# Kernel optimization log

Measured on AMD Instinct MI355X. Metric: run time of the kernel, lower is better.

Reference implementation:

```python
import jax, jax.numpy as jnp
import numpy as np

VERTS = [5023, 1256, 314, 79, 20]
SPIRAL_LEN = 9
T_FRAMES = 32
LATENT = 64


def _spiral_conv(x, idx, W, b):
    # x: [B, N, C]; idx: [N, L]; gather spiral neighborhoods then linear
    B = x.shape[0]
    g = x[:, idx.reshape(-1), :].reshape(B, idx.shape[0], -1)  # [B, N, L*C]
    return g @ W.T + b


def _pool(x, rows, cols, vals, n_out):
    # sparse matmul: out[b, rows] += x[b, cols] * vals  (index_select + scatter_add)
    gathered = x[:, cols, :] * vals[None, :, None]
    return jnp.zeros((x.shape[0], n_out, x.shape[2]), x.dtype).at[:, rows, :].add(gathered)


def _lstm_dir(x, Wih, Whh, bih, bhh, reverse):
    # x: [T, B, D]; PyTorch gate order i, f, g, o
    Bz, H = x.shape[1], Whh.shape[1]
    bias = bih + bhh
    def step(carry, xt):
        h, c = carry
        g = xt @ Wih.T + h @ Whh.T + bias
        i, f, gg, o = jnp.split(g, 4, axis=-1)
        c = jax.nn.sigmoid(f) * c + jax.nn.sigmoid(i) * jnp.tanh(gg)
        h = jax.nn.sigmoid(o) * jnp.tanh(c)
        return (h, c), h
    init = (jnp.zeros((Bz, H), x.dtype), jnp.zeros((Bz, H), x.dtype))
    _, hs = jax.lax.scan(step, init, x, reverse=reverse)
    return hs


def _forward(audio_hidden, vertices, actor,
             sp_idx0, sp_idx1, sp_idx2, sp_idx3,
             d0_rows, d0_cols, d0_vals, d1_rows, d1_cols, d1_vals,
             d2_rows, d2_cols, d2_vals, d3_rows, d3_cols, d3_vals,
             u0_rows, u0_cols, u0_vals, u1_rows, u1_cols, u1_vals,
             u2_rows, u2_cols, u2_vals, u3_rows, u3_cols, u3_vals,
             enc_W0, enc_b0, enc_W1, enc_b1, enc_W2, enc_b2, enc_W3, enc_b3,
             enc_lin_W, enc_lin_b, dec_lin_W, dec_lin_b,
             dec_W0, dec_b0, dec_W1, dec_b1, dec_W2, dec_b2, dec_W3, dec_b3,
             dec_W4, dec_b4, aud_W, aud_b,
             l0_Wih, l0_Whh, l0_bih, l0_bhh, l12_Wih, l12_Whh, l12_bih, l12_bhh):
    ah = audio_hidden
    if ah.shape[1] % 2 != 0:
        ah = ah[:, :ah.shape[1] - 1]
    tv = vertices.shape[1]
    if ah.shape[1] > 2 * tv:
        ah = ah[:, :2 * tv]
    elif ah.shape[1] < 2 * tv:
        tv = ah.shape[1] // 2
    hs = ah.reshape(1, ah.shape[1] // 2, ah.shape[2] * 2)[:, :tv]  # [1, T, 1536]
    audio_emb = hs @ aud_W.T + aud_b                                # [1, T, LATENT]
    # --- mesh encoder on actor template: (spiral conv -> ELU -> down pool) x4 -> Linear ---
    sp = (sp_idx0, sp_idx1, sp_idx2, sp_idx3)
    down = ((d0_rows, d0_cols, d0_vals), (d1_rows, d1_cols, d1_vals),
            (d2_rows, d2_cols, d2_vals), (d3_rows, d3_cols, d3_vals))
    encp = ((enc_W0, enc_b0), (enc_W1, enc_b1), (enc_W2, enc_b2), (enc_W3, enc_b3))
    x = actor
    for i in range(4):
        x = jax.nn.elu(_spiral_conv(x, sp[i], *encp[i]))
        x = _pool(x, *down[i], VERTS[i + 1])
    z = x.reshape(x.shape[0], -1) @ enc_lin_W.T + enc_lin_b        # [1, LATENT]
    actor_emb = jnp.broadcast_to(z[:, None, :], audio_emb.shape)
    # --- 3-layer bidirectional LSTM ---
    h = jnp.concatenate([audio_emb, actor_emb], axis=-1).transpose(1, 0, 2)  # [T, 1, 2*LATENT]
    for layer in range(3):
        if layer == 0:
            Wih, Whh, bih, bhh = l0_Wih, l0_Whh, l0_bih, l0_bhh
        else:
            Wih, Whh, bih, bhh = l12_Wih[layer - 1], l12_Whh[layer - 1], l12_bih[layer - 1], l12_bhh[layer - 1]
        f = _lstm_dir(h, Wih[0], Whh[0], bih[0], bhh[0], False)
        r = _lstm_dir(h, Wih[1], Whh[1], bih[1], bhh[1], True)
        h = jnp.concatenate([f, r], axis=-1)
    latent = h.transpose(1, 0, 2)[0]                               # [T, LATENT]
    # --- mesh decoder, batched over all frames (replaces the python per-frame loop) ---
    up = ((u0_rows, u0_cols, u0_vals), (u1_rows, u1_cols, u1_vals),
          (u2_rows, u2_cols, u2_vals), (u3_rows, u3_cols, u3_vals))
    decp = ((dec_W0, dec_b0), (dec_W1, dec_b1), (dec_W2, dec_b2), (dec_W3, dec_b3))
    y = latent @ dec_lin_W.T + dec_lin_b                           # [T, 20*256]
    y = y.reshape(y.shape[0], VERTS[4], -1)                        # [T, 20, 256]
    for i in range(4):
        j = 3 - i
        y = _pool(y, *up[j], VERTS[j])
        y = jax.nn.elu(_spiral_conv(y, sp[j], *decp[i]))
    y = _spiral_conv(y, sp[0], dec_W4, dec_b4)                     # [T, 5023, 3]
    return y + actor                                               # broadcast residual, == vstacked preds


def setup_inputs() -> dict:
    key = jax.random.key(0)
    ks = iter(jax.random.split(key, 96))
    def nrm(shape, s=0.05):
        return jax.random.normal(next(ks), shape, jnp.float32) * s
    def rint(shape, hi):
        return jax.random.randint(next(ks), shape, 0, hi)
    inp = {}
    inp['audio_hidden'] = nrm((1, 2 * T_FRAMES, 768), 1.0)
    inp['vertices'] = nrm((1, T_FRAMES, VERTS[0], 3), 1.0)
    inp['actor'] = nrm((1, VERTS[0], 3), 1.0)
    for i in range(4):
        inp['sp_idx%d' % i] = rint((VERTS[i], SPIRAL_LEN), VERTS[i])
    for i in range(4):
        nnz = 3 * VERTS[i + 1]
        inp['d%d_rows' % i] = rint((nnz,), VERTS[i + 1])
        inp['d%d_cols' % i] = rint((nnz,), VERTS[i])
        inp['d%d_vals' % i] = jax.random.uniform(next(ks), (nnz,), jnp.float32)
    for i in range(4):
        nnz = 3 * VERTS[i]
        inp['u%d_rows' % i] = rint((nnz,), VERTS[i])
        inp['u%d_cols' % i] = rint((nnz,), VERTS[i + 1])
        inp['u%d_vals' % i] = jax.random.uniform(next(ks), (nnz,), jnp.float32)
    OC = [32, 64, 128, 256]
    ic = 3
    for i in range(4):
        inp['enc_W%d' % i] = nrm((OC[i], ic * SPIRAL_LEN))
        inp['enc_b%d' % i] = nrm((OC[i],))
        ic = OC[i]
    inp['enc_lin_W'] = nrm((LATENT, VERTS[4] * OC[3]))
    inp['enc_lin_b'] = nrm((LATENT,))
    inp['dec_lin_W'] = nrm((VERTS[4] * OC[3], LATENT))
    inp['dec_lin_b'] = nrm((VERTS[4] * OC[3],))
    dic = [256, 256, 128, 64]
    doc = [256, 128, 64, 32]
    for i in range(4):
        inp['dec_W%d' % i] = nrm((doc[i], dic[i] * SPIRAL_LEN))
        inp['dec_b%d' % i] = nrm((doc[i],))
    inp['dec_W4'] = nrm((3, OC[0] * SPIRAL_LEN))
    inp['dec_b4'] = nrm((3,))
    inp['aud_W'] = nrm((LATENT, 1536))
    inp['aud_b'] = nrm((LATENT,))
    H = LATENT // 2
    inp['l0_Wih'] = nrm((2, 4 * H, 2 * LATENT))
    inp['l0_Whh'] = nrm((2, 4 * H, H))
    inp['l0_bih'] = nrm((2, 4 * H))
    inp['l0_bhh'] = nrm((2, 4 * H))
    inp['l12_Wih'] = nrm((2, 2, 4 * H, 2 * H))
    inp['l12_Whh'] = nrm((2, 2, 4 * H, H))
    inp['l12_bih'] = nrm((2, 2, 4 * H))
    inp['l12_bhh'] = nrm((2, 2, 4 * H))
    return inp


def reference(audio_hidden, vertices, actor,
              sp_idx0, sp_idx1, sp_idx2, sp_idx3,
              d0_rows, d0_cols, d0_vals, d1_rows, d1_cols, d1_vals,
              d2_rows, d2_cols, d2_vals, d3_rows, d3_cols, d3_vals,
              u0_rows, u0_cols, u0_vals, u1_rows, u1_cols, u1_vals,
              u2_rows, u2_cols, u2_vals, u3_rows, u3_cols, u3_vals,
              enc_W0, enc_b0, enc_W1, enc_b1, enc_W2, enc_b2, enc_W3, enc_b3,
              enc_lin_W, enc_lin_b, dec_lin_W, dec_lin_b,
              dec_W0, dec_b0, dec_W1, dec_b1, dec_W2, dec_b2, dec_W3, dec_b3,
              dec_W4, dec_b4, aud_W, aud_b,
              l0_Wih, l0_Whh, l0_bih, l0_bhh, l12_Wih, l12_Whh, l12_bih, l12_bhh):
    return _forward(audio_hidden, vertices, actor,
                    sp_idx0, sp_idx1, sp_idx2, sp_idx3,
                    d0_rows, d0_cols, d0_vals, d1_rows, d1_cols, d1_vals,
                    d2_rows, d2_cols, d2_vals, d3_rows, d3_cols, d3_vals,
                    u0_rows, u0_cols, u0_vals, u1_rows, u1_cols, u1_vals,
                    u2_rows, u2_cols, u2_vals, u3_rows, u3_cols, u3_vals,
                    enc_W0, enc_b0, enc_W1, enc_b1, enc_W2, enc_b2, enc_W3, enc_b3,
                    enc_lin_W, enc_lin_b, dec_lin_W, dec_lin_b,
                    dec_W0, dec_b0, dec_W1, dec_b1, dec_W2, dec_b2, dec_W3, dec_b3,
                    dec_W4, dec_b4, aud_W, aud_b,
                    l0_Wih, l0_Whh, l0_bih, l0_bhh, l12_Wih, l12_Whh, l12_bih, l12_bhh)
```

## Files before the change

kernel.cpp:

```cpp
#include <hip/hip_runtime.h>
#include <cstdint>
#include <cstddef>


typedef unsigned short u16;
typedef __attribute__((ext_vector_type(8))) short short8;
typedef __attribute__((ext_vector_type(4))) float float4v;
#define CDIV(a,b) (((a)+(b)-1)/(b))
#define POOL_CAP 64

__device__ __forceinline__ float bf(u16 u){ return __uint_as_float(((unsigned)u)<<16); }
__device__ __forceinline__ u16 fb(float x){
  unsigned u = __float_as_uint(x);
  unsigned r = u + 0x7fffu + ((u>>16)&1u);
  return (u16)(r>>16);
}
__device__ __forceinline__ float lo16(unsigned u){ return __uint_as_float(u<<16); }
__device__ __forceinline__ float hi16(unsigned u){ return __uint_as_float(u & 0xffff0000u); }

struct WCast { const float* src[7]; int cum[8]; };
struct Lists {
  const int* rows[8];
  int nnz[8];
  int curoff[8];
  int lstoff[8];
};

__global__ void __launch_bounds__(256) setup_k(
    Lists L, int totN, int NF, int* __restrict__ curBase, int* __restrict__ lstBase,
    WCast C, int totW, int NC, u16* __restrict__ Wbf,
    const float* __restrict__ audio, const float* __restrict__ audW,
    const float* __restrict__ audB, float* __restrict__ h0,
    const int* __restrict__ u3rows, const int* __restrict__ u3cols,
    const float* __restrict__ u3vals,
    const float* __restrict__ dlW, const float* __restrict__ dlb,
    float* __restrict__ M, float* __restrict__ bp, int NM){
  int blk = blockIdx.x;
  int tid = threadIdx.x;
  if (blk < NF){
    int i = blk*256 + tid;
    if (i < totN){
      int off = i, k = 0;
      while (off >= L.nnz[k]){ off -= L.nnz[k]; k++; }
      int r = L.rows[k][off];
      int p = atomicAdd(curBase + L.curoff[k] + r, 1);
      if (p < POOL_CAP) lstBase[L.lstoff[k] + r*POOL_CAP + p] = off;
    }
    return;
  }
  blk -= NF;
  if (blk < NC){
    int i = blk*256 + tid;
    if (i < totW){
      int k = 0;
      while (i >= C.cum[k+1]) k++;
      Wbf[i] = fb(C.src[k][i - C.cum[k]]);
    }
    return;
  }
  blk -= NC;
  if (blk < 32){
    int t = blk;
    int f = tid >> 2, sl = tid & 3;
    const float4* x4 = (const float4*)(audio + t*1536);
    const float4* w4 = (const float4*)(audW + f*1536);
    float acc = 0.f;
    for (int k=sl; k<384; k+=4){
      float4 xv = x4[k], wv = w4[k];
      acc += xv.x*wv.x + xv.y*wv.y + xv.z*wv.z + xv.w*wv.w;
    }
    acc += __shfl_down(acc, 2, 64);
    acc += __shfl_down(acc, 1, 64);
    if (sl == 0) h0[t*128 + f] = acc + audB[f];
    return;
  }
  blk -= 32;
  if (blk < NM){
    int i = blk*256 + tid;
    if (i >= 79*256*16) return;
    int k4 = i & 15; int rc = i >> 4;
    int c = rc & 255; int r = rc >> 8;
    float4 acc = {0.f,0.f,0.f,0.f};
    for (int e=0; e<237; ++e){
      if (u3rows[e] == r){
        float v = u3vals[e];
        float4 w = *(const float4*)(dlW + ((size_t)(u3cols[e]*256 + c))*64 + k4*4);
        acc.x += v*w.x; acc.y += v*w.y; acc.z += v*w.z; acc.w += v*w.w;
      }
    }
    *(float4*)(M + (size_t)rc*64 + k4*4) = acc;
    return;
  }
  blk -= NM;
  int i = blk*256 + tid;
  if (i >= 79*256) return;
  int c = i & 255; int r = i >> 8;
  float acc = 0.f;
  for (int e=0; e<237; ++e)
    if (u3rows[e] == r) acc += u3vals[e]*dlb[u3cols[e]*256 + c];
  bp[i] = acc;
}

__global__ void __launch_bounds__(256) fs1_k(
    const float* __restrict__ x, const int* __restrict__ sp,
    const int* __restrict__ cols, const float* __restrict__ vals,
    const int* __restrict__ cur, const int* __restrict__ lst,
    const float* __restrict__ W, const float* __restrict__ bias,
    u16* __restrict__ out){
  int i = blockIdx.x*256 + threadIdx.x;
  if (i >= 1256*32) return;
  int c = i & 31, r = i >> 5;
  int deg = cur[r]; if (deg > POOL_CAP) deg = POOL_CAP;
  const int* le = lst + r*POOL_CAP;
  float bc = bias[c];
  const float* wc = W + (size_t)c*27;
  float acc = 0.f;
  for (int k=0;k<deg;k++){
    int e = le[k];
    float v = vals[e];
    const int* vix = sp + cols[e]*9;
    float s = bc;
    #pragma unroll
    for (int j=0;j<9;j++){
      const float* xr = x + (size_t)vix[j]*3;
      s += xr[0]*wc[j*3] + xr[1]*wc[j*3+1] + xr[2]*wc[j*3+2];
    }
    if (s < 0.f) s = expm1f(s);
    acc += v*s;
  }
  out[i] = fb(acc);
}

template<int IC, int BN, int BM>
__global__ void __launch_bounds__(256) conv_mfma(
    const u16* __restrict__ x, const int* __restrict__ idx,
    const u16* __restrict__ Wb, const float* __restrict__ bias,
    u16* __restrict__ out, int V, int OC, int M){
  constexpr int K = 9*IC;
  constexpr int KC = K/32;
  constexpr int NT = BN/16;
  constexpr int MT = BM/64;
  constexpr int LOG2 = (IC==32?5: IC==64?6: IC==128?7:8);
  constexpr int AST = 40;
  __shared__ u16 Asm[2][BM*AST];
  __shared__ u16 Bsm[2][BN*AST];
  __shared__ int rowB[BM], rowV[BM];
  __shared__ int sidx[BM*9];
  int t = threadIdx.x;
  int m0 = blockIdx.x*BM;
  int o0 = blockIdx.y*BN;
  if (t < BM){
    int mg = m0 + t;
    if (mg < M){ int b = mg / V; rowB[t] = b; rowV[t] = mg - b*V; }
    else rowB[t] = -1;
  }
  __syncthreads();
  for (int i=t; i<BM*9; i+=256){
    int r = i/9, s = i - r*9;
    sidx[i] = (rowB[r] >= 0) ? idx[rowV[r]*9 + s] : 0;
  }
  int lane = t & 63, wave = t >> 6;
  int quad = lane >> 4, col = lane & 15;
  float4v acc[MT][NT];
  #pragma unroll
  for (int mi=0;mi<MT;mi++)
    #pragma unroll
    for (int nt=0;nt<NT;nt++) acc[mi][nt] = (float4v)0.f;

  uint4 aval[MT]; uint4 bval;
  auto fetch = [&](int kc){
    int s  = (kc*32) >> LOG2;
    int c0 = (kc*32) & (IC-1);
    #pragma unroll
    for (int rpt=0; rpt<MT; ++rpt){
      int seg = t + 256*rpt;
      int arow = seg >> 2, aq = seg & 3;
      int b = rowB[arow];
      uint4 v = {0u,0u,0u,0u};
      if (b >= 0){
        int ix = sidx[arow*9 + s];
        v = *(const uint4*)(x + ((size_t)b*V + ix)*IC + c0 + aq*8);
      }
      aval[rpt] = v;
    }
    if (t < BN*4){
      int br = t >> 2, bq = t & 3;
      bval = *(const uint4*)(Wb + (size_t)(o0+br)*K + kc*32 + bq*8);
    }
  };

  __syncthreads();
  fetch(0);

  for (int kc = 0; kc < KC; ++kc){
    int buf = kc & 1;
    #pragma unroll
    for (int rpt=0; rpt<MT; ++rpt){
      int seg = t + 256*rpt;
      int arow = seg >> 2, aq = seg & 3;
      *(uint4*)&Asm[buf][arow*AST + aq*8] = aval[rpt];
    }
    if (t < BN*4){
      int br = t >> 2, bq = t & 3;
      *(uint4*)&Bsm[buf][br*AST + bq*8] = bval;
    }
    __syncthreads();
    if (kc+1 < KC) fetch(kc+1);
    short8 a[MT];
    #pragma unroll
    for (int mi=0;mi<MT;mi++)
      a[mi] = *(const short8*)&Asm[buf][(wave*MT*16 + mi*16 + col)*AST + quad*8];
    #pragma unroll
    for (int nt=0; nt<NT; ++nt){
      short8 bfr = *(const short8*)&Bsm[buf][(nt*16 + col)*AST + quad*8];
      #pragma unroll
      for (int mi=0;mi<MT;mi++)
        acc[mi][nt] = __builtin_amdgcn_mfma_f32_16x16x32_bf16(a[mi], bfr, acc[mi][nt], 0, 0, 0);
    }
  }
  #pragma unroll
  for (int mi=0;mi<MT;mi++){
    #pragma unroll
    for (int nt=0; nt<NT; ++nt){
      int o = o0 + nt*16 + col;
      float bv = bias[o];
      #pragma unroll
      for (int r=0;r<4;r++){
        int mg = m0 + wave*MT*16 + mi*16 + quad*4 + r;
        if (mg < M){
          float val = acc[mi][nt][r] + bv;
          if (val < 0.f) val = expm1f(val);
          out[(size_t)mg*OC + o] = fb(val);
        }
      }
    }
  }
}

__global__ void pool_g8_k(const u16* __restrict__ x, const int* __restrict__ cols,
                          const float* __restrict__ vals, const int* __restrict__ cur,
                          const int* __restrict__ lst, u16* __restrict__ out,
                          int B, int Vin, int Vout, int C){
  int C8 = C >> 3;
  int total = B*Vout*C8;
  int i = blockIdx.x*blockDim.x + threadIdx.x;
  if (i >= total) return;
  int c8 = i % C8; int tt = i / C8; int r = tt % Vout; int b = tt / Vout;
  int deg = cur[r]; if (deg > POOL_CAP) deg = POOL_CAP;
  const int* le = lst + r*POOL_CAP;
  float a0=0.f,a1=0.f,a2=0.f,a3=0.f,a4=0.f,a5=0.f,a6=0.f,a7=0.f;
  for (int k=0;k<deg;k++){
    int e = le[k];
    float v = vals[e];
    uint4 xv = *(const uint4*)(x + ((size_t)b*Vin + (size_t)cols[e])*C + c8*8);
    a0 += v*lo16(xv.x); a1 += v*hi16(xv.x);
    a2 += v*lo16(xv.y); a3 += v*hi16(xv.y);
    a4 += v*lo16(xv.z); a5 += v*hi16(xv.z);
    a6 += v*lo16(xv.w); a7 += v*hi16(xv.w);
  }
  uint4 o;
  o.x = ((unsigned)fb(a0)) | (((unsigned)fb(a1))<<16);
  o.y = ((unsigned)fb(a2)) | (((unsigned)fb(a3))<<16);
  o.z = ((unsigned)fb(a4)) | (((unsigned)fb(a5))<<16);
  o.w = ((unsigned)fb(a6)) | (((unsigned)fb(a7))<<16);
  *(uint4*)(out + ((size_t)b*Vout + (size_t)r)*C + c8*8) = o;
}

__global__ void __launch_bounds__(256) enc_lin_k(
    const u16* __restrict__ x, const float* __restrict__ W,
    const float* __restrict__ b, float* __restrict__ h0){
  int f = blockIdx.x;
  int t = threadIdx.x;
  const ushort4* x4 = (const ushort4*)x;
  const float4* w4 = (const float4*)(W + (size_t)f*5120);
  float acc = 0.f;
  for (int k=t; k<1280; k+=256){
    ushort4 xv = x4[k]; float4 wv = w4[k];
    acc += bf(xv.x)*wv.x + bf(xv.y)*wv.y + bf(xv.z)*wv.z + bf(xv.w)*wv.w;
  }
  #pragma unroll
  for (int off=32; off; off>>=1) acc += __shfl_down(acc, off, 64);
  __shared__ float red[4];
  if ((t & 63) == 0) red[t>>6] = acc;
  __syncthreads();
  if (t < 32){
    float zf = b[f] + red[0] + red[1] + red[2] + red[3];
    h0[t*128 + 64 + f] = zf;
  }
}

__device__ __forceinline__ float sigm(float x){ return 1.f/(1.f+__expf(-x)); }
__device__ __forceinline__ float tanhfast(float x){ return 1.f - 2.f/(__expf(2.f*x)+1.f); }

__global__ void __launch_bounds__(256) lstm3_k(
    const float* __restrict__ h0,
    const float* __restrict__ l0_Wih, const float* __restrict__ l0_Whh,
    const float* __restrict__ l0_bih, const float* __restrict__ l0_bhh,
    const float* __restrict__ l12_Wih, const float* __restrict__ l12_Whh,
    const float* __restrict__ l12_bih, const float* __restrict__ l12_bhh,
    float* __restrict__ latent){
  __shared__ __align__(16) u16 xb[32*136];
  __shared__ __align__(16) float xp[2*32*128];
  __shared__ __align__(16) u16 obuf[32*64];
  __shared__ __align__(16) float hsh32[2][32];
  __shared__ float bias_l[256];
  int t = threadIdx.x;
  int lane = t & 63, wave = t >> 6;
  int quad = lane >> 4, col = lane & 15;

  for (int i=t;i<32*128;i+=256){ int tt=i>>7, k=i&127; xb[tt*136+k]=fb(h0[i]); }

  for (int layer=0; layer<3; layer++){
    int IN = (layer==0)?128:64;
    const float *Wih,*Whh,*bih,*bhh;
    if (layer==0){ Wih=l0_Wih; Whh=l0_Whh; bih=l0_bih; bhh=l0_bhh; }
    else {
      int mb=(layer-1)*2;
      Wih=l12_Wih + (size_t)mb*128*64; Whh=l12_Whh + (size_t)mb*128*32;
      bih=l12_bih + mb*128; bhh=l12_bhh + mb*128;
    }
    bias_l[t] = bih[(t>>7)*128 + (t&127)] + bhh[(t>>7)*128 + (t&127)];
    __syncthreads();

    {
      int dirA = wave >> 1, o0 = (wave & 1)*64;
      const float* WA = Wih + (size_t)dirA*128*IN;
      float4v acc[2][4];
      #pragma unroll
      for (int mi=0;mi<2;mi++)
        #pragma unroll
        for (int nt=0;nt<4;nt++) acc[mi][nt] = (float4v)0.f;
      for (int kc=0; kc<IN/32; ++kc){
        short8 bfrag[4];
        #pragma unroll
        for (int nt=0;nt<4;nt++){
          const float* src = WA + (size_t)(o0+nt*16+col)*IN + kc*32 + quad*8;
          float4 w0 = *(const float4*)src;
          float4 w1 = *(const float4*)(src+4);
          alignas(16) u16 tmp[8] = {fb(w0.x),fb(w0.y),fb(w0.z),fb(w0.w),
                                    fb(w1.x),fb(w1.y),fb(w1.z),fb(w1.w)};
          bfrag[nt] = *(const short8*)tmp;
        }
        short8 afrag[2];
        #pragma unroll
        for (int mi=0;mi<2;mi++)
          afrag[mi] = *(const short8*)&xb[(mi*16+col)*136 + kc*32 + quad*8];
        #pragma unroll
        for (int nt=0;nt<4;nt++)
          #pragma unroll
          for (int mi=0;mi<2;mi++)
            acc[mi][nt] = __builtin_amdgcn_mfma_f32_16x16x32_bf16(afrag[mi], bfrag[nt], acc[mi][nt], 0, 0, 0);
      }
      #pragma unroll
      for (int mi=0;mi<2;mi++)
        #pragma unroll
        for (int nt=0;nt<4;nt++){
          int j = o0 + nt*16 + col;
          float bv = bias_l[dirA*128 + j];
          #pragma unroll
          for (int r=0;r<4;r++){
            int tt = mi*16 + quad*4 + r;
            xp[dirA*4096 + tt*128 + j] = acc[mi][nt][r] + bv;
          }
        }
    }
    __syncthreads();

    if (wave < 2){
      int dir = wave; bool rev = (dir == 1);
      int unit = lane & 31, gh = lane >> 5;
      int jA = gh*32 + unit;
      int jB = (gh+2)*32 + unit;
      const float* WD = Whh + (size_t)dir*128*32;
      float wA[32], wB[32];
      #pragma unroll
      for (int k=0;k<32;k++){ wA[k]=WD[(size_t)jA*32+k]; wB[k]=WD[(size_t)jB*32+k]; }
      float* hsd = &hsh32[dir][0];
      if (gh==0) hsd[unit] = 0.f;
      float creg = 0.f;
      const float* xpd = xp + dir*4096;
      float gAc = xpd[(rev?31:0)*128 + jA];
      float gBc = xpd[(rev?31:0)*128 + jB];
      #pragma unroll 1
      for (int s=0;s<32;s++){
        int tx = rev ? (31-s) : s;
        int sn = (s+1 < 32) ? s+1 : 31;
        int txn = rev ? (31-sn) : sn;
        float gA2 = xpd[txn*128 + jA];
        float gB2 = xpd[txn*128 + jB];
        const float4* h4 = (const float4*)hsd;
        float a0=0.f,a1=0.f,a2=0.f,a3=0.f,b0=0.f,b1=0.f,b2=0.f,b3=0.f;
        #pragma unroll
        for (int k=0;k<8;k++){
          float4 hv = h4[k];
          a0=fmaf(hv.x,wA[4*k+0],a0); b0=fmaf(hv.x,wB[4*k+0],b0);
          a1=fmaf(hv.y,wA[4*k+1],a1); b1=fmaf(hv.y,wB[4*k+1],b1);
          a2=fmaf(hv.z,wA[4*k+2],a2); b2=fmaf(hv.z,wB[4*k+2],b2);
          a3=fmaf(hv.w,wA[4*k+3],a3); b3=fmaf(hv.w,wB[4*k+3],b3);
        }
        float gA = gAc + ((a0+a1)+(a2+a3));
        float gB = gBc + ((b0+b1)+(b2+b3));
        float actA = sigm(gA);
        float tB = sigm(gh ? gB : 2.f*gB);
        float actB = gh ? tB : (2.f*tB - 1.f);
        float pA = __shfl_xor(actA, 32, 64);
        float pB = __shfl_xor(actB, 32, 64);
        float gi = gh ? pA : actA;
        float gf = gh ? actA : pA;
        float gg = gh ? pB : actB;
        float go = gh ? actB : pB;
        float cn = fmaf(gf, creg, gi*gg);
        float hn = go * tanhfast(cn);
        creg = cn;
        if (gh==0){
          hsd[unit] = hn;
          obuf[tx*64 + dir*32 + unit] = fb(hn);
        }
        gAc = gA2; gBc = gB2;
      }
    }
    __syncthreads();
    if (layer < 2){
      for (int i=t;i<32*64;i+=256){ int tt=i>>6, k=i&63; xb[tt*136+k]=obuf[i]; }
      __syncthreads();
    }
  }
  for (int i=t;i<32*64;i+=256) latent[i] = bf(obuf[i]);
}

__global__ void __launch_bounds__(256) dlp_k(
    const float* __restrict__ latent, const float* __restrict__ M,
    const float* __restrict__ bp, u16* __restrict__ y){
  __shared__ float mt[64][65];
  __shared__ float lt[32][64];
  int tid = threadIdx.x;
  int r = blockIdx.x % 79;
  int c0 = (blockIdx.x / 79) * 64;
  for (int i=tid; i<2048; i+=256) lt[i>>6][i&63] = latent[i];
  const float* Msrc = M + ((size_t)r*256 + c0)*64;
  for (int i=tid; i<4096; i+=256) mt[i>>6][i&63] = Msrc[i];
  __syncthreads();
  int cl = tid & 63;
  int tg = tid >> 6;
  float bpv = bp[r*256 + c0 + cl];
  #pragma unroll 1
  for (int p=0; p<8; ++p){
    int t = p*4 + tg;
    float acc = bpv;
    #pragma unroll 16
    for (int k=0;k<64;k++) acc += lt[t][k]*mt[cl][k];
    y[((size_t)t*79 + r)*256 + c0 + cl] = fb(acc);
  }
}

__global__ void final_k(const u16* __restrict__ x, const int* __restrict__ idx,
                        const float* __restrict__ W, const float* __restrict__ bias,
                        const float* __restrict__ actor, float* __restrict__ out){
  __shared__ float Wsm[3*288];
  __shared__ float bsm[3];
  int t = threadIdx.x;
  for (int i=t;i<864;i+=256) Wsm[i]=W[i];
  if (t<3) bsm[t]=bias[t];
  __syncthreads();
  int g = blockIdx.x*256 + t;
  if (g >= 32*5023) return;
  int v = g % 5023, b = g / 5023;
  const u16* xb = x + (size_t)b*5023*32;
  const int* vix = idx + v*9;
  float a0=bsm[0], a1=bsm[1], a2=bsm[2];
  for (int s=0;s<9;s++){
    const ushort4* xr = (const ushort4*)(xb + (size_t)vix[s]*32);
    #pragma unroll
    for (int k=0;k<8;k++){
      ushort4 xv = xr[k];
      float x0=bf(xv.x), x1=bf(xv.y), x2=bf(xv.z), x3=bf(xv.w);
      int kk = s*32 + k*4;
      a0 += x0*Wsm[kk] + x1*Wsm[kk+1] + x2*Wsm[kk+2] + x3*Wsm[kk+3];
      a1 += x0*Wsm[288+kk] + x1*Wsm[288+kk+1] + x2*Wsm[288+kk+2] + x3*Wsm[288+kk+3];
      a2 += x0*Wsm[576+kk] + x1*Wsm[576+kk+1] + x2*Wsm[576+kk+2] + x3*Wsm[576+kk+3];
    }
  }
  out[(size_t)g*3+0] = a0 + actor[v*3+0];
  out[(size_t)g*3+1] = a1 + actor[v*3+1];
  out[(size_t)g*3+2] = a2 + actor[v*3+2];
}

extern "C" void kernel_launch(void* const* d_in, const int* in_sizes, int n_in,
                              void* d_out, int out_size, void* d_ws, size_t ws_size,
                              hipStream_t stream){
  (void)in_sizes; (void)n_in; (void)out_size; (void)ws_size;

  const float* audio = (const float*)d_in[0];
  const float* actor = (const float*)d_in[2];
  const int* sp[4]   = {(const int*)d_in[3],(const int*)d_in[4],(const int*)d_in[5],(const int*)d_in[6]};
  const int* drows[4]; const int* dcols[4]; const float* dvals[4];
  for (int i=0;i<4;i++){ drows[i]=(const int*)d_in[7+3*i]; dcols[i]=(const int*)d_in[8+3*i]; dvals[i]=(const float*)d_in[9+3*i]; }
  const int* urows[4]; const int* ucols[4]; const float* uvals[4];
  for (int i=0;i<4;i++){ urows[i]=(const int*)d_in[19+3*i]; ucols[i]=(const int*)d_in[20+3*i]; uvals[i]=(const float*)d_in[21+3*i]; }
  const float* encW[4]={(const float*)d_in[31],(const float*)d_in[33],(const float*)d_in[35],(const float*)d_in[37]};
  const float* encB[4]={(const float*)d_in[32],(const float*)d_in[34],(const float*)d_in[36],(const float*)d_in[38]};
  const float* enc_lin_W=(const float*)d_in[39]; const float* enc_lin_b=(const float*)d_in[40];
  const float* dec_lin_W=(const float*)d_in[41]; const float* dec_lin_b=(const float*)d_in[42];
  const float* decW[5]={(const float*)d_in[43],(const float*)d_in[45],(const float*)d_in[47],(const float*)d_in[49],(const float*)d_in[51]};
  const float* decB[5]={(const float*)d_in[44],(const float*)d_in[46],(const float*)d_in[48],(const float*)d_in[50],(const float*)d_in[52]};
  const float* audW=(const float*)d_in[53]; const float* audB=(const float*)d_in[54];
  const float* l0_Wih=(const float*)d_in[55]; const float* l0_Whh=(const float*)d_in[56];
  const float* l0_bih=(const float*)d_in[57]; const float* l0_bhh=(const float*)d_in[58];
  const float* l12_Wih=(const float*)d_in[59]; const float* l12_Whh=(const float*)d_in[60];
  const float* l12_bih=(const float*)d_in[61]; const float* l12_bhh=(const float*)d_in[62];
  float* out = (float*)d_out;

  char* base = (char*)d_ws;
  u16* A  = (u16*)base;
  u16* Bb = (u16*)(base + 10287104);
  int* curBase = (int*)(base + 30891520);
  int* lstBase = (int*)(base + 30924928);
  u16* Wbf = (u16*)(base + 33060224);
  float* sm = (float*)(base + 35788160);
  float* h0     = sm;
  float* latent = sm + 4096;
  float* Mf = (float*)(base + 4194304);
  float* bp = (float*)(base + 9437184);

  const int wsz[7] = {64*288, 128*576, 256*1152, 256*2304, 128*2304, 64*1152, 32*576};
  WCast WC; int wcum = 0;
  const float* wsrc[7] = {encW[1],encW[2],encW[3],decW[0],decW[1],decW[2],decW[3]};
  int wo[7];
  for (int k=0;k<7;k++){ WC.src[k]=wsrc[k]; WC.cum[k]=wcum; wo[k]=wcum; wcum+=wsz[k]; }
  WC.cum[7]=wcum;

  const int pVout[8] = {1256,314,79,20,5023,1256,314,79};
  const int pNnz[8]  = {3768,942,237,60,15069,3768,942,237};
  Lists L; int curoff=0, lstoff=0, totnnz=0;
  const int* prow[8] = {drows[0],drows[1],drows[2],drows[3],urows[0],urows[1],urows[2],urows[3]};
  int curo[8], lsto[8];
  for (int k=0;k<8;k++){
    L.rows[k]=prow[k]; L.nnz[k]=pNnz[k];
    L.curoff[k]=curoff; L.lstoff[k]=lstoff;
    curo[k]=curoff; lsto[k]=lstoff;
    curoff += pVout[k]; lstoff += pVout[k]*POOL_CAP; totnnz += pNnz[k];
  }
  hipMemsetAsync(curBase, 0, (size_t)curoff*4, stream);

  int NF = CDIV(totnnz,256), NC = CDIV(wcum,256);
  int NM = CDIV(79*256*16,256), NB = CDIV(79*256,256);
  setup_k<<<NF+NC+32+NM+NB,256,0,stream>>>(L, totnnz, NF, curBase, lstBase,
                                           WC, wcum, NC, Wbf,
                                           audio, audW, audB, h0,
                                           urows[3], ucols[3], uvals[3],
                                           dec_lin_W, dec_lin_b, Mf, bp, NM);

  fs1_k<<<CDIV(1256*32,256),256,0,stream>>>(
      actor, sp[0], dcols[0], dvals[0], curBase+curo[0], lstBase+lsto[0],
      encW[0], encB[0], Bb);
  conv_mfma<32,64,64><<<dim3(CDIV(1256,64),1),256,0,stream>>>(Bb, sp[1], Wbf+wo[0], encB[1], A, 1256, 64, 1256);
  pool_g8_k<<<CDIV(314*8,256),256,0,stream>>>(A, dcols[1], dvals[1], curBase+curo[1], lstBase+lsto[1], Bb, 1, 1256, 314, 64);
  conv_mfma<64,64,64><<<dim3(CDIV(314,64),2),256,0,stream>>>(Bb, sp[2], Wbf+wo[1], encB[2], A, 314, 128, 314);
  pool_g8_k<<<CDIV(79*16,256),256,0,stream>>>(A, dcols[2], dvals[2], curBase+curo[2], lstBase+lsto[2], Bb, 1, 314, 79, 128);
  conv_mfma<128,64,64><<<dim3(CDIV(79,64),4),256,0,stream>>>(Bb, sp[3], Wbf+wo[2], encB[3], A, 79, 256, 79);
  pool_g8_k<<<CDIV(20*32,256),256,0,stream>>>(A, dcols[3], dvals[3], curBase+curo[3], lstBase+lsto[3], Bb, 1, 79, 20, 256);
  enc_lin_k<<<64,256,0,stream>>>(Bb, enc_lin_W, enc_lin_b, h0);

  lstm3_k<<<1,256,0,stream>>>(h0, l0_Wih, l0_Whh, l0_bih, l0_bhh,
                              l12_Wih, l12_Whh, l12_bih, l12_bhh, latent);

  dlp_k<<<79*4,256,0,stream>>>(latent, Mf, bp, Bb);
  conv_mfma<256,64,64><<<dim3(CDIV(2528,64),4),256,0,stream>>>(Bb, sp[3], Wbf+wo[3], decB[0], A, 79, 256, 2528);

  pool_g8_k<<<CDIV(32*314*32,256),256,0,stream>>>(A, ucols[2], uvals[2], curBase+curo[6], lstBase+lsto[6], Bb, 32, 79, 314, 256);
  conv_mfma<256,64,64><<<dim3(CDIV(10048,64),2),256,0,stream>>>(Bb, sp[2], Wbf+wo[4], decB[1], A, 314, 128, 10048);

  pool_g8_k<<<CDIV(32*1256*16,256),256,0,stream>>>(A, ucols[1], uvals[1], curBase+curo[5], lstBase+lsto[5], Bb, 32, 314, 1256, 128);
  conv_mfma<128,64,128><<<dim3(CDIV(40192,128),1),256,0,stream>>>(Bb, sp[1], Wbf+wo[5], decB[2], A, 1256, 64, 40192);

  pool_g8_k<<<CDIV(32*5023*8,256),256,0,stream>>>(A, ucols[0], uvals[0], curBase+curo[4], lstBase+lsto[4], Bb, 32, 1256, 5023, 64);
  conv_mfma<64,32,128><<<dim3(CDIV(160736,128),1),256,0,stream>>>(Bb, sp[0], Wbf+wo[6], decB[3], A, 5023, 32, 160736);

  final_k<<<CDIV(32*5023,256),256,0,stream>>>(A, sp[0], decW[4], decB[4], actor, out);
}
```

Before: 567.5 us.

## Fuse encoder downsampling pools into the following spiral convolution kernels

Adds a conv_pl_k kernel in which each block first computes the sparse downsampling pool of its input into shared memory and then runs the MFMA spiral convolution from that buffer. For the deepest layer it also applies the next pool in shared memory and writes only the pooled result. This removes three separate pool launches and their global round-trips in the encoder. In exchange every block recomputes the full pooled input redundantly, and the fused output pool goes to an offset inside Bb so it does not overwrite the conv input.

```diff
diff --git a/kernel.cpp b/kernel.cpp
--- a/kernel.cpp
+++ b/kernel.cpp
@@ -233,6 +233,164 @@
           out[(size_t)mg*OC + o] = fb(val);
         }
       }
+    }
+  }
+}
+
+template<int IC, int BN, int BM, int VP, bool OPOOL, int VQ>
+__global__ void __launch_bounds__(256) conv_pl_k(
+    const u16* __restrict__ x,
+    const int* __restrict__ pcols, const float* __restrict__ pvals,
+    const int* __restrict__ pcur, const int* __restrict__ plst,
+    const int* __restrict__ idx,
+    const u16* __restrict__ Wb, const float* __restrict__ bias,
+    u16* __restrict__ out, int OC,
+    const int* __restrict__ qcols, const float* __restrict__ qvals,
+    const int* __restrict__ qcur, const int* __restrict__ qlst,
+    u16* __restrict__ out2){
+  constexpr int K = 9*IC;
+  constexpr int KC = K/32;
+  constexpr int NT = BN/16;
+  constexpr int MT = BM/64;
+  constexpr int LOG2 = (IC==64?6: IC==128?7:8);
+  constexpr int AST = 40;
+  constexpr int OST = BN + 8;
+  constexpr int M = VP;
+  __shared__ __align__(16) u16 P[VP*IC];
+  __shared__ u16 Asm[2][BM*AST];
+  __shared__ u16 Bsm[2][BN*AST];
+  __shared__ int sidx[BM*9];
+  __shared__ __align__(16) u16 OutT[OPOOL ? VP*OST : 16];
+  int t = threadIdx.x;
+  int m0 = blockIdx.x*BM;
+  int o0 = blockIdx.y*BN;
+
+  constexpr int C8 = IC/8;
+  for (int i=t; i<VP*C8; i+=256){
+    int c8 = i % C8, r = i / C8;
+    int deg = pcur[r]; if (deg > POOL_CAP) deg = POOL_CAP;
+    const int* le = plst + r*POOL_CAP;
+    float a0=0.f,a1=0.f,a2=0.f,a3=0.f,a4=0.f,a5=0.f,a6=0.f,a7=0.f;
+    for (int k=0;k<deg;k++){
+      int e = le[k];
+      float v = pvals[e];
+      uint4 xv = *(const uint4*)(x + (size_t)pcols[e]*IC + c8*8);
+      a0 += v*lo16(xv.x); a1 += v*hi16(xv.x);
+      a2 += v*lo16(xv.y); a3 += v*hi16(xv.y);
+      a4 += v*lo16(xv.z); a5 += v*hi16(xv.z);
+      a6 += v*lo16(xv.w); a7 += v*hi16(xv.w);
+    }
+    uint4 o;
+    o.x = ((unsigned)fb(a0)) | (((unsigned)fb(a1))<<16);
+    o.y = ((unsigned)fb(a2)) | (((unsigned)fb(a3))<<16);
+    o.z = ((unsigned)fb(a4)) | (((unsigned)fb(a5))<<16);
+    o.w = ((unsigned)fb(a6)) | (((unsigned)fb(a7))<<16);
+    *(uint4*)&P[r*IC + c8*8] = o;
+  }
+  for (int i=t; i<BM*9; i+=256){
+    int r = i/9, s = i - r*9;
+    sidx[i] = (m0 + r < M) ? idx[(m0+r)*9 + s] : 0;
+  }
+  int lane = t & 63, wave = t >> 6;
+  int quad = lane >> 4, col = lane & 15;
+  float4v acc[MT][NT];
+  #pragma unroll
+  for (int mi=0;mi<MT;mi++)
+    #pragma unroll
+    for (int nt=0;nt<NT;nt++) acc[mi][nt] = (float4v)0.f;
+
+  uint4 aval[MT]; uint4 bval;
+  auto fetch = [&](int kc){
+    int s  = (kc*32) >> LOG2;
+    int c0 = (kc*32) & (IC-1);
+    #pragma unroll
+    for (int rpt=0; rpt<MT; ++rpt){
+      int seg = t + 256*rpt;
+      int arow = seg >> 2, aq = seg & 3;
+      uint4 v = {0u,0u,0u,0u};
+      if (m0 + arow < M){
+        int ix = sidx[arow*9 + s];
+        v = *(const uint4*)&P[ix*IC + c0 + aq*8];
+      }
+      aval[rpt] = v;
+    }
+    if (t < BN*4){
+      int br = t >> 2, bq = t & 3;
+      bval = *(const uint4*)(Wb + (size_t)(o0+br)*K + kc*32 + bq*8);
+    }
+  };
+
+  __syncthreads();
+  fetch(0);
+
+  for (int kc = 0; kc < KC; ++kc){
+    int buf = kc & 1;
+    #pragma unroll
+    for (int rpt=0; rpt<MT; ++rpt){
+      int seg = t + 256*rpt;
+      int arow = seg >> 2, aq = seg & 3;
+      *(uint4*)&Asm[buf][arow*AST + aq*8] = aval[rpt];
+    }
+    if (t < BN*4){
+      int br = t >> 2, bq = t & 3;
+      *(uint4*)&Bsm[buf][br*AST + bq*8] = bval;
+    }
+    __syncthreads();
+    if (kc+1 < KC) fetch(kc+1);
+    short8 a[MT];
+    #pragma unroll
+    for (int mi=0;mi<MT;mi++)
+      a[mi] = *(const short8*)&Asm[buf][(wave*MT*16 + mi*16 + col)*AST + quad*8];
+    #pragma unroll
+    for (int nt=0; nt<NT; ++nt){
+      short8 bfr = *(const short8*)&Bsm[buf][(nt*16 + col)*AST + quad*8];
+      #pragma unroll
+      for (int mi=0;mi<MT;mi++)
+        acc[mi][nt] = __builtin_amdgcn_mfma_f32_16x16x32_bf16(a[mi], bfr, acc[mi][nt], 0, 0, 0);
+    }
+  }
+  #pragma unroll
+  for (int mi=0;mi<MT;mi++){
+    #pragma unroll
+    for (int nt=0; nt<NT; ++nt){
+      int o = o0 + nt*16 + col;
+      float bv = bias[o];
+      #pragma unroll
+      for (int r=0;r<4;r++){
+        int mg = m0 + wave*MT*16 + mi*16 + quad*4 + r;
+        if (mg < M){
+          float val = acc[mi][nt][r] + bv;
+          if (val < 0.f) val = expm1f(val);
+          u16 hb = fb(val);
+          if constexpr (OPOOL) OutT[mg*OST + nt*16 + col] = hb;
+          else out[(size_t)mg*OC + o] = hb;
+        }
+      }
+    }
+  }
+  if constexpr (OPOOL){
+    __syncthreads();
+    constexpr int QC8 = BN/8;
+    for (int i=t; i<VQ*QC8; i+=256){
+      int c8 = i % QC8, q = i / QC8;
+      int deg = qcur[q]; if (deg > POOL_CAP) deg = POOL_CAP;
+      const int* le = qlst + q*POOL_CAP;
+      float a0=0.f,a1=0.f,a2=0.f,a3=0.f,a4=0.f,a5=0.f,a6=0.f,a7=0.f;
+      for (int k=0;k<deg;k++){
+        int e = le[k];
+        float v = qvals[e];
+        uint4 xv = *(const uint4*)&OutT[qcols[e]*OST + c8*8];
+        a0 += v*lo16(xv.x); a1 += v*hi16(xv.x);
+        a2 += v*lo16(xv.y); a3 += v*hi16(xv.y);
+        a4 += v*lo16(xv.z); a5 += v*hi16(xv.z);
+        a6 += v*lo16(xv.w); a7 += v*hi16(xv.w);
+      }
+      uint4 o;
+      o.x = ((unsigned)fb(a0)) | (((unsigned)fb(a1))<<16);
+      o.y = ((unsigned)fb(a2)) | (((unsigned)fb(a3))<<16);
+      o.z = ((unsigned)fb(a4)) | (((unsigned)fb(a5))<<16);
+      o.w = ((unsigned)fb(a6)) | (((unsigned)fb(a7))<<16);
+      *(uint4*)(out2 + (size_t)q*OC + o0 + c8*8) = o;
     }
   }
 }
@@ -554,12 +712,15 @@
       actor, sp[0], dcols[0], dvals[0], curBase+curo[0], lstBase+lsto[0],
       encW[0], encB[0], Bb);
   conv_mfma<32,64,64><<<dim3(CDIV(1256,64),1),256,0,stream>>>(Bb, sp[1], Wbf+wo[0], encB[1], A, 1256, 64, 1256);
-  pool_g8_k<<<CDIV(314*8,256),256,0,stream>>>(A, dcols[1], dvals[1], curBase+curo[1], lstBase+lsto[1], Bb, 1, 1256, 314, 64);
-  conv_mfma<64,64,64><<<dim3(CDIV(314,64),2),256,0,stream>>>(Bb, sp[2], Wbf+wo[1], encB[2], A, 314, 128, 314);
-  pool_g8_k<<<CDIV(79*16,256),256,0,stream>>>(A, dcols[2], dvals[2], curBase+curo[2], lstBase+lsto[2], Bb, 1, 314, 79, 128);
-  conv_mfma<128,64,64><<<dim3(CDIV(79,64),4),256,0,stream>>>(Bb, sp[3], Wbf+wo[2], encB[3], A, 79, 256, 79);
-  pool_g8_k<<<CDIV(20*32,256),256,0,stream>>>(A, dcols[3], dvals[3], curBase+curo[3], lstBase+lsto[3], Bb, 1, 79, 20, 256);
-  enc_lin_k<<<64,256,0,stream>>>(Bb, enc_lin_W, enc_lin_b, h0);
+  conv_pl_k<64,64,64,314,false,1><<<dim3(CDIV(314,64),2),256,0,stream>>>(
+      A, dcols[1], dvals[1], curBase+curo[1], lstBase+lsto[1],
+      sp[2], Wbf+wo[1], encB[2], Bb, 128,
+      nullptr, nullptr, nullptr, nullptr, nullptr);
+  conv_pl_k<128,64,128,79,true,20><<<dim3(1,4),256,0,stream>>>(
+      Bb, dcols[2], dvals[2], curBase+curo[2], lstBase+lsto[2],
+      sp[3], Wbf+wo[2], encB[3], nullptr, 256,
+      dcols[3], dvals[3], curBase+curo[3], lstBase+lsto[3], Bb + 65536);
+  enc_lin_k<<<64,256,0,stream>>>(Bb + 65536, enc_lin_W, enc_lin_b, h0);
 
   lstm3_k<<<1,256,0,stream>>>(h0, l0_Wih, l0_Whh, l0_bih, l0_bhh,
                               l12_Wih, l12_Whh, l12_bih, l12_bhh, latent);
```

After: 618.8 us. 1.09x slower.
